# Performance work log

Hardware: AMD Instinct MI355X
Metric: run time of the kernel (lower is better)

The kernel has to match this reference:

```python
import jax, jax.numpy as jnp
import numpy as np

N_NODES = 50000
N_EDGES = 800000
D = 64
N_REL = 16


def setup_inputs() -> dict:
    key = jax.random.key(0)
    ks = jax.random.split(key, 8)
    return {
        "nfeat": jax.random.normal(ks[0], (N_NODES, D), dtype=jnp.float32),
        "efeat": jax.random.normal(ks[1], (N_EDGES, D), dtype=jnp.float32),
        "relation_W": jax.random.normal(ks[2], (N_REL, D, D), dtype=jnp.float32) * (1.0 / np.sqrt(D)),
        "W1": jax.random.normal(ks[3], (D, D), dtype=jnp.float32) * (1.0 / np.sqrt(D)),
        "W2": jax.random.normal(ks[4], (D, D), dtype=jnp.float32) * (1.0 / np.sqrt(D)),
        "src": jax.random.randint(ks[5], (N_EDGES,), 0, N_NODES, dtype=jnp.int32),
        "dst": jax.random.randint(ks[6], (N_EDGES,), 0, N_NODES, dtype=jnp.int32),
        "etype": jax.random.randint(ks[7], (N_EDGES,), 0, N_REL, dtype=jnp.int32),
    }


def _leaky_relu(x, slope=0.01):
    return jnp.where(x >= 0, x, slope * x)


def reference(nfeat, efeat, relation_W, W1, W2, src, dst, etype):
    N, Din = nfeat.shape
    R, _, Dr = relation_W.shape
    # W_r h for every (relation, node) pair, then gather per-edge.
    # Mathematically identical to per-edge bmm_maybe_select, but avoids the
    # (E, Din, Dr) per-edge weight materialization.
    proj = jnp.einsum('nd,rde->rne', nfeat, relation_W).reshape(R * N, Dr)  # (R*N, Dr)
    flat_src = etype * N + src
    flat_dst = etype * N + dst
    t_r = proj[flat_src]  # (E, Dr) == W_r h_t
    h_r = proj[flat_dst]  # (E, Dr) == W_r h_h
    # att = (W_r h_t)^T tanh(W_r h_h + e_r)
    att = jnp.sum(t_r * jnp.tanh(h_r + efeat), axis=-1)  # (E,)
    # edge softmax grouped by destination node
    seg_max = jax.ops.segment_max(att, dst, num_segments=N)  # (N,)
    ex = jnp.exp(att - seg_max[dst])
    denom = jax.ops.segment_sum(ex, dst, num_segments=N)  # (N,)
    a = ex / denom[dst]  # (E,)
    # u_mul_e + sum scatter aggregation
    h_neighbor = jax.ops.segment_sum(nfeat[src] * a[:, None], dst, num_segments=N)  # (N, Din)
    # Bi-interaction residual
    out = _leaky_relu((nfeat + h_neighbor) @ W1) + _leaky_relu((nfeat * h_neighbor) @ W2)
    return (h_neighbor, out)
```

## Files before the change

kernel.cpp:

```cpp
#include <hip/hip_runtime.h>
#include <math.h>


#define DIM 64
#define PA 72

typedef _Float16 half8 __attribute__((ext_vector_type(8)));
typedef float f32x4 __attribute__((ext_vector_type(4)));
typedef unsigned int u32x4 __attribute__((ext_vector_type(4)));

__device__ __forceinline__ float4 f4zero() { return make_float4(0.f, 0.f, 0.f, 0.f); }

__device__ __forceinline__ unsigned short f2bf(float x) {
    unsigned u = __float_as_uint(x);
    u += 0x7FFFu + ((u >> 16) & 1u);
    return (unsigned short)(u >> 16);
}

__device__ __forceinline__ float fast_tanh(float x) {
    float ex = __expf(2.0f * x);
    return 1.0f - 2.0f / (ex + 1.0f);
}

__device__ __forceinline__ void bf8up(u32x4 u, float* f) {
    f[0] = __uint_as_float(u[0] << 16);
    f[1] = __uint_as_float(u[0] & 0xFFFF0000u);
    f[2] = __uint_as_float(u[1] << 16);
    f[3] = __uint_as_float(u[1] & 0xFFFF0000u);
    f[4] = __uint_as_float(u[2] << 16);
    f[5] = __uint_as_float(u[2] & 0xFFFF0000u);
    f[6] = __uint_as_float(u[3] << 16);
    f[7] = __uint_as_float(u[3] & 0xFFFF0000u);
}

__global__ __launch_bounds__(256) void k_proj(const float* __restrict__ nfeat,
                                              const float* __restrict__ relW,
                                              unsigned short* __restrict__ proj,
                                              int N, int R) {
    __shared__ _Float16 shA[64 * PA];
    __shared__ _Float16 shB[64 * PA];

    const int tx = threadIdx.x;
    const int n0 = blockIdx.x * 64;

    const float4* nf4 = (const float4*)(nfeat + (size_t)n0 * DIM);
#pragma unroll
    for (int i = 0; i < 4; ++i) {
        int idx = tx + 256 * i;
        int row = idx >> 4, c = idx & 15;
        float4 v = (n0 + row < N) ? nf4[idx] : f4zero();
        _Float16* p = &shA[row * PA + c * 4];
        p[0] = (_Float16)v.x; p[1] = (_Float16)v.y;
        p[2] = (_Float16)v.z; p[3] = (_Float16)v.w;
    }
    __syncthreads();

    const int w = tx >> 6;
    const int lane = tx & 63;
    const int lm = lane & 15;
    const int lq = lane >> 4;
    const int m0 = w * 16;

    half8 a0 = *(const half8*)&shA[(m0 + lm) * PA + 0 * 32 + lq * 8];
    half8 a1 = *(const half8*)&shA[(m0 + lm) * PA + 1 * 32 + lq * 8];

    for (int r = 0; r < R; ++r) {
        __syncthreads();
        const float4* Wr4 = (const float4*)(relW + (size_t)r * DIM * DIM);
#pragma unroll
        for (int i = 0; i < 4; ++i) {
            int idx = tx + 256 * i;
            int d = idx >> 4, c = (idx & 15) * 4;
            float4 v = Wr4[idx];
            shB[(c + 0) * PA + d] = (_Float16)v.x;
            shB[(c + 1) * PA + d] = (_Float16)v.y;
            shB[(c + 2) * PA + d] = (_Float16)v.z;
            shB[(c + 3) * PA + d] = (_Float16)v.w;
        }
        __syncthreads();

        f32x4 acc[4];
#pragma unroll
        for (int ct = 0; ct < 4; ++ct) {
            half8 b0 = *(const half8*)&shB[(ct * 16 + lm) * PA + 0 * 32 + lq * 8];
            half8 b1 = *(const half8*)&shB[(ct * 16 + lm) * PA + 1 * 32 + lq * 8];
            f32x4 c = {0.f, 0.f, 0.f, 0.f};
            c = __builtin_amdgcn_mfma_f32_16x16x32_f16(a0, b0, c, 0, 0, 0);
            c = __builtin_amdgcn_mfma_f32_16x16x32_f16(a1, b1, c, 0, 0, 0);
            acc[ct] = c;
        }

        unsigned short* projR = proj + ((size_t)r * N + n0) * DIM;
#pragma unroll
        for (int ct = 0; ct < 4; ++ct) {
#pragma unroll
            for (int i = 0; i < 4; ++i) {
                int row = m0 + lq * 4 + i;
                int col = ct * 16 + lm;
                if (n0 + row < N)
                    projR[(size_t)row * DIM + col] = f2bf(acc[ct][i]);
            }
        }
    }
}

__global__ __launch_bounds__(256) void k_hist(const int* __restrict__ dst,
                                              int* __restrict__ deg, int E) {
    int e = blockIdx.x * 256 + threadIdx.x;
    if (e < E) atomicAdd(&deg[dst[e]], 1);
}

__global__ __launch_bounds__(256) void k_scan1(const int* __restrict__ deg,
                                               int* __restrict__ bsum, int N) {
    __shared__ int sh[256];
    int i = blockIdx.x * 256 + threadIdx.x;
    int t = threadIdx.x;
    sh[t] = (i < N) ? deg[i] : 0;
    __syncthreads();
#pragma unroll
    for (int s = 128; s > 0; s >>= 1) {
        if (t < s) sh[t] += sh[t + s];
        __syncthreads();
    }
    if (t == 0) bsum[blockIdx.x] = sh[0];
}

__global__ __launch_bounds__(256) void k_scan2(int* __restrict__ bsum, int nb,
                                               int* __restrict__ offN, int E) {
    __shared__ int sh[256];
    int t = threadIdx.x;
    int v = (t < nb) ? bsum[t] : 0;
    sh[t] = v;
    __syncthreads();
#pragma unroll
    for (int d = 1; d < 256; d <<= 1) {
        int o = (t >= d) ? sh[t - d] : 0;
        __syncthreads();
        sh[t] += o;
        __syncthreads();
    }
    if (t < nb) bsum[t] = sh[t] - v;
    if (t == 0) offN[0] = E;
}

__global__ __launch_bounds__(256) void k_scan3(const int* __restrict__ deg,
                                               const int* __restrict__ bsum,
                                               int* __restrict__ off,
                                               int* __restrict__ cursor, int N) {
    __shared__ int sh[256];
    int i = blockIdx.x * 256 + threadIdx.x;
    int t = threadIdx.x;
    int v = (i < N) ? deg[i] : 0;
    sh[t] = v;
    __syncthreads();
#pragma unroll
    for (int d = 1; d < 256; d <<= 1) {
        int o = (t >= d) ? sh[t - d] : 0;
        __syncthreads();
        sh[t] += o;
        __syncthreads();
    }
    if (i < N) {
        int pre = bsum[blockIdx.x] + sh[t] - v;
        off[i] = pre;
        cursor[i] = pre;
    }
}

__global__ __launch_bounds__(256) void k_fill(const int* __restrict__ dst,
                                              const int* __restrict__ src,
                                              int* __restrict__ cursor,
                                              int* __restrict__ pos,
                                              int* __restrict__ src_s, int E) {
    int e = blockIdx.x * 256 + threadIdx.x;
    if (e >= E) return;
    int p = atomicAdd(&cursor[dst[e]], 1);
    pos[e] = p;
    src_s[p] = src[e];
}

__global__ __launch_bounds__(256) void k_att(const unsigned short* __restrict__ proj,
                                             const float* __restrict__ efeat,
                                             const int* __restrict__ src,
                                             const int* __restrict__ dst,
                                             const int* __restrict__ etype,
                                             const int* __restrict__ pos,
                                             float* __restrict__ att_s,
                                             int N, int E) {
    int t = blockIdx.x * 256 + threadIdx.x;
    int e = t >> 3;
    int sub = t & 7;
    if (e >= E) return;
    int s = src[e], d = dst[e], r = etype[e];

    const u32x4* tp = (const u32x4*)(proj + ((size_t)((unsigned)(r * N + s))) * DIM) + sub;
    const u32x4* hp = (const u32x4*)(proj + ((size_t)((unsigned)(r * N + d))) * DIM) + sub;
    const f32x4* ef = (const f32x4*)(efeat + (size_t)e * DIM) + sub * 2;

    u32x4 tu = *tp;
    u32x4 hu = *hp;
    f32x4 efa = __builtin_nontemporal_load(ef);
    f32x4 efb = __builtin_nontemporal_load(ef + 1);

    float tf[8], hf[8];
    bf8up(tu, tf);
    bf8up(hu, hf);
    float ev[8] = {efa[0], efa[1], efa[2], efa[3], efb[0], efb[1], efb[2], efb[3]};

    float dotv = 0.f;
#pragma unroll
    for (int i = 0; i < 8; ++i)
        dotv = fmaf(tf[i], fast_tanh(hf[i] + ev[i]), dotv);

    dotv += __shfl_xor(dotv, 1);
    dotv += __shfl_xor(dotv, 2);
    dotv += __shfl_xor(dotv, 4);

    if (sub == 0) att_s[pos[e]] = dotv;
}

__global__ __launch_bounds__(256) void k_aggB(const float* __restrict__ att_s,
                                              const int* __restrict__ src_s,
                                              const float* __restrict__ nfeat,
                                              const int* __restrict__ off,
                                              const float* __restrict__ W1,
                                              const float* __restrict__ W2,
                                              float* __restrict__ hn,
                                              float* __restrict__ out,
                                              int N) {
    const int node = blockIdx.x * 4 + (threadIdx.x >> 6);
    if (node >= N) return;
    const int lane = threadIdx.x & 63;

    const int jb = off[node];
    const int je = off[node + 1];

    float m = -INFINITY;
    for (int j0 = jb; j0 < je; j0 += 64) {
        int j = j0 + lane;
        float a = (j < je) ? att_s[j] : -INFINITY;
        m = fmaxf(m, a);
    }
#pragma unroll
    for (int ms = 32; ms; ms >>= 1) m = fmaxf(m, __shfl_xor(m, ms));

    float pl = 0.f, acc = 0.f, acc2 = 0.f;
    for (int j0 = jb; j0 < je; j0 += 64) {
        int j = j0 + lane;
        int cnt = min(64, je - j0);
        float a = (j < je) ? att_s[j] : -INFINITY;
        float p = __expf(a - m);
        int s = (j < je) ? src_s[j] : 0;
        pl += p;
        int jj = 0;
        for (; jj + 3 < cnt; jj += 4) {
            float pj0 = __shfl(p, jj + 0);
            float pj1 = __shfl(p, jj + 1);
            float pj2 = __shfl(p, jj + 2);
            float pj3 = __shfl(p, jj + 3);
            int sj0 = __shfl(s, jj + 0);
            int sj1 = __shfl(s, jj + 1);
            int sj2 = __shfl(s, jj + 2);
            int sj3 = __shfl(s, jj + 3);
            float x0 = nfeat[(size_t)sj0 * DIM + lane];
            float x1 = nfeat[(size_t)sj1 * DIM + lane];
            float x2 = nfeat[(size_t)sj2 * DIM + lane];
            float x3 = nfeat[(size_t)sj3 * DIM + lane];
            acc  = fmaf(pj0, x0, acc);
            acc2 = fmaf(pj1, x1, acc2);
            acc  = fmaf(pj2, x2, acc);
            acc2 = fmaf(pj3, x3, acc2);
        }
        for (; jj < cnt; ++jj) {
            float pj = __shfl(p, jj);
            int sj = __shfl(s, jj);
            acc = fmaf(pj, nfeat[(size_t)sj * DIM + lane], acc);
        }
    }
    acc += acc2;
#pragma unroll
    for (int ms = 32; ms; ms >>= 1) pl += __shfl_xor(pl, ms);

    const float hval = (je > jb) ? acc / pl : 0.f;
    hn[(size_t)node * DIM + lane] = hval;

    const float nf = nfeat[(size_t)node * DIM + lane];
    const float v1 = nf + hval;
    const float v2 = nf * hval;
    float o1 = 0.f, o2 = 0.f;
#pragma unroll 8
    for (int d = 0; d < DIM; ++d) {
        float s1 = __shfl(v1, d);
        float s2 = __shfl(v2, d);
        o1 = fmaf(s1, W1[d * DIM + lane], o1);
        o2 = fmaf(s2, W2[d * DIM + lane], o2);
    }
    out[(size_t)node * DIM + lane] =
        (o1 >= 0.f ? o1 : 0.01f * o1) + (o2 >= 0.f ? o2 : 0.01f * o2);
}

extern "C" void kernel_launch(void* const* d_in, const int* in_sizes, int n_in,
                              void* d_out, int out_size, void* d_ws, size_t ws_size,
                              hipStream_t stream) {
    const float* nfeat = (const float*)d_in[0];
    const float* efeat = (const float*)d_in[1];
    const float* relW  = (const float*)d_in[2];
    const float* W1    = (const float*)d_in[3];
    const float* W2    = (const float*)d_in[4];
    const int* src   = (const int*)d_in[5];
    const int* dst   = (const int*)d_in[6];
    const int* etype = (const int*)d_in[7];

    const int N = in_sizes[0] / DIM;
    const int E = in_sizes[5];
    const int R = in_sizes[2] / (DIM * DIM);
    const int NB = (N + 255) / 256;

    float* out = (float*)d_out;
    float* hn  = out;
    float* bi  = out + (size_t)N * DIM;

    unsigned short* proj = (unsigned short*)d_ws;
    size_t projElems = (size_t)R * N * DIM;
    int* deg    = (int*)(proj + projElems);
    int* off    = deg + N;
    int* cursor = off + (N + 1);
    int* bsum   = cursor + N;
    int* pos    = bsum + 256;
    int* src_s  = pos + E;
    float* att_s = (float*)(src_s + E);

    (void)hipMemsetAsync(deg, 0, (size_t)N * sizeof(int), stream);

    k_hist<<<(E + 255) / 256, 256, 0, stream>>>(dst, deg, E);
    k_scan1<<<NB, 256, 0, stream>>>(deg, bsum, N);
    k_scan2<<<1, 256, 0, stream>>>(bsum, NB, off + N, E);
    k_scan3<<<NB, 256, 0, stream>>>(deg, bsum, off, cursor, N);
    k_fill<<<(E + 255) / 256, 256, 0, stream>>>(dst, src, cursor, pos, src_s, E);

    k_proj<<<(N + 63) / 64, 256, 0, stream>>>(nfeat, relW, proj, N, R);

    k_att<<<((size_t)E * 8 + 255) / 256, 256, 0, stream>>>(proj, efeat, src, dst, etype,
                                                           pos, att_s, N, E);

    k_aggB<<<(N + 3) / 4, 256, 0, stream>>>(att_s, src_s, nfeat, off,
                                            W1, W2, hn, bi, N);
}
```

Measured before the change: 567.3 us.

## Fuse CSR fill into histogram ranks, coalesce proj stores, cache bi-interaction weights in LDS

New measurement: 568.2 us. Within noise of the previous version (+0.2%).

```diff
diff --git a/kernel.cpp b/kernel.cpp
--- a/kernel.cpp
+++ b/kernel.cpp
@@ -39,6 +39,7 @@
                                               int N, int R) {
     __shared__ _Float16 shA[64 * PA];
     __shared__ _Float16 shB[64 * PA];
+    unsigned short* shSt = (unsigned short*)shA;
 
     const int tx = threadIdx.x;
     const int n0 = blockIdx.x * 64;
@@ -90,63 +91,39 @@
             acc[ct] = c;
         }
 
-        unsigned short* projR = proj + ((size_t)r * N + n0) * DIM;
 #pragma unroll
         for (int ct = 0; ct < 4; ++ct) {
 #pragma unroll
             for (int i = 0; i < 4; ++i) {
                 int row = m0 + lq * 4 + i;
                 int col = ct * 16 + lm;
-                if (n0 + row < N)
-                    projR[(size_t)row * DIM + col] = f2bf(acc[ct][i]);
+                shSt[row * PA + col] = f2bf(acc[ct][i]);
             }
         }
+        __syncthreads();
+
+        unsigned short* projR = proj + ((size_t)r * N + n0) * DIM;
+#pragma unroll
+        for (int k = 0; k < 2; ++k) {
+            int chunk = tx + k * 256;
+            int row = chunk >> 3, cc = chunk & 7;
+            uint4 v = *(const uint4*)&shSt[row * PA + cc * 8];
+            if (n0 + row < N)
+                *(uint4*)&projR[(size_t)row * DIM + cc * 8] = v;
+        }
     }
 }
 
 __global__ __launch_bounds__(256) void k_hist(const int* __restrict__ dst,
-                                              int* __restrict__ deg, int E) {
+                                              int* __restrict__ deg,
+                                              int* __restrict__ rank, int E) {
     int e = blockIdx.x * 256 + threadIdx.x;
-    if (e < E) atomicAdd(&deg[dst[e]], 1);
+    if (e < E) rank[e] = atomicAdd(&deg[dst[e]], 1);
 }
 
 __global__ __launch_bounds__(256) void k_scan1(const int* __restrict__ deg,
+                                               int* __restrict__ epart,
                                                int* __restrict__ bsum, int N) {
-    __shared__ int sh[256];
-    int i = blockIdx.x * 256 + threadIdx.x;
-    int t = threadIdx.x;
-    sh[t] = (i < N) ? deg[i] : 0;
-    __syncthreads();
-#pragma unroll
-    for (int s = 128; s > 0; s >>= 1) {
-        if (t < s) sh[t] += sh[t + s];
-        __syncthreads();
-    }
-    if (t == 0) bsum[blockIdx.x] = sh[0];
-}
-
-__global__ __launch_bounds__(256) void k_scan2(int* __restrict__ bsum, int nb,
-                                               int* __restrict__ offN, int E) {
-    __shared__ int sh[256];
-    int t = threadIdx.x;
-    int v = (t < nb) ? bsum[t] : 0;
-    sh[t] = v;
-    __syncthreads();
-#pragma unroll
-    for (int d = 1; d < 256; d <<= 1) {
-        int o = (t >= d) ? sh[t - d] : 0;
-        __syncthreads();
-        sh[t] += o;
-        __syncthreads();
-    }
-    if (t < nb) bsum[t] = sh[t] - v;
-    if (t == 0) offN[0] = E;
-}
-
-__global__ __launch_bounds__(256) void k_scan3(const int* __restrict__ deg,
-                                               const int* __restrict__ bsum,
-                                               int* __restrict__ off,
-                                               int* __restrict__ cursor, int N) {
     __shared__ int sh[256];
     int i = blockIdx.x * 256 + threadIdx.x;
     int t = threadIdx.x;
@@ -160,23 +137,36 @@
         sh[t] += o;
         __syncthreads();
     }
-    if (i < N) {
-        int pre = bsum[blockIdx.x] + sh[t] - v;
-        off[i] = pre;
-        cursor[i] = pre;
-    }
-}
-
-__global__ __launch_bounds__(256) void k_fill(const int* __restrict__ dst,
-                                              const int* __restrict__ src,
-                                              int* __restrict__ cursor,
-                                              int* __restrict__ pos,
-                                              int* __restrict__ src_s, int E) {
-    int e = blockIdx.x * 256 + threadIdx.x;
-    if (e >= E) return;
-    int p = atomicAdd(&cursor[dst[e]], 1);
-    pos[e] = p;
-    src_s[p] = src[e];
+    if (i < N) epart[i] = sh[t] - v;
+    if (t == 255) bsum[blockIdx.x] = sh[255];
+}
+
+__global__ __launch_bounds__(1024) void k_scan2(const int* __restrict__ epart,
+                                                const int* __restrict__ bsum,
+                                                int nb,
+                                                int* __restrict__ off,
+                                                int N, int E) {
+    __shared__ int bx[256];
+    int t = threadIdx.x;
+    int v = 0;
+    if (t < 256) {
+        v = (t < nb) ? bsum[t] : 0;
+        bx[t] = v;
+    }
+    __syncthreads();
+#pragma unroll
+    for (int d = 1; d < 256; d <<= 1) {
+        int o = 0;
+        if (t < 256 && t >= d) o = bx[t - d];
+        __syncthreads();
+        if (t < 256) bx[t] += o;
+        __syncthreads();
+    }
+    if (t < 256) bx[t] -= v;
+    __syncthreads();
+    for (int i = t; i < N; i += 1024)
+        off[i] = epart[i] + bx[i >> 8];
+    if (t == 0) off[N] = E;
 }
 
 __global__ __launch_bounds__(256) void k_att(const unsigned short* __restrict__ proj,
@@ -184,8 +174,10 @@
                                              const int* __restrict__ src,
                                              const int* __restrict__ dst,
                                              const int* __restrict__ etype,
-                                             const int* __restrict__ pos,
+                                             const int* __restrict__ rank,
+                                             const int* __restrict__ off,
                                              float* __restrict__ att_s,
+                                             int* __restrict__ src_s,
                                              int N, int E) {
     int t = blockIdx.x * 256 + threadIdx.x;
     int e = t >> 3;
@@ -216,7 +208,9 @@
     dotv += __shfl_xor(dotv, 2);
     dotv += __shfl_xor(dotv, 4);
 
-    if (sub == 0) att_s[pos[e]] = dotv;
+    int p = off[d] + rank[e];
+    if (sub == 0) att_s[p] = dotv;
+    if (sub == 1) src_s[p] = s;
 }
 
 __global__ __launch_bounds__(256) void k_aggB(const float* __restrict__ att_s,
@@ -228,9 +222,24 @@
                                               float* __restrict__ hn,
                                               float* __restrict__ out,
                                               int N) {
-    const int node = blockIdx.x * 4 + (threadIdx.x >> 6);
+    __shared__ float shW[2][DIM * DIM];
+    const int tx = threadIdx.x;
+    {
+        const float4* w14 = (const float4*)W1;
+        const float4* w24 = (const float4*)W2;
+        float4* s0 = (float4*)shW[0];
+        float4* s1 = (float4*)shW[1];
+#pragma unroll
+        for (int i = 0; i < 4; ++i) {
+            s0[tx + 256 * i] = w14[tx + 256 * i];
+            s1[tx + 256 * i] = w24[tx + 256 * i];
+        }
+    }
+    __syncthreads();
+
+    const int node = blockIdx.x * 4 + (tx >> 6);
     if (node >= N) return;
-    const int lane = threadIdx.x & 63;
+    const int lane = tx & 63;
 
     const int jb = off[node];
     const int je = off[node + 1];
@@ -292,8 +301,8 @@
     for (int d = 0; d < DIM; ++d) {
         float s1 = __shfl(v1, d);
         float s2 = __shfl(v2, d);
-        o1 = fmaf(s1, W1[d * DIM + lane], o1);
-        o2 = fmaf(s2, W2[d * DIM + lane], o2);
+        o1 = fmaf(s1, shW[0][d * DIM + lane], o1);
+        o2 = fmaf(s2, shW[1][d * DIM + lane], o2);
     }
     out[(size_t)node * DIM + lane] =
         (o1 >= 0.f ? o1 : 0.01f * o1) + (o2 >= 0.f ? o2 : 0.01f * o2);
@@ -324,24 +333,22 @@
     size_t projElems = (size_t)R * N * DIM;
     int* deg    = (int*)(proj + projElems);
     int* off    = deg + N;
-    int* cursor = off + (N + 1);
-    int* bsum   = cursor + N;
-    int* pos    = bsum + 256;
-    int* src_s  = pos + E;
+    int* epart  = off + (N + 1);
+    int* bsum   = epart + N;
+    int* rank   = bsum + 256;
+    int* src_s  = rank + E;
     float* att_s = (float*)(src_s + E);
 
     (void)hipMemsetAsync(deg, 0, (size_t)N * sizeof(int), stream);
 
-    k_hist<<<(E + 255) / 256, 256, 0, stream>>>(dst, deg, E);
-    k_scan1<<<NB, 256, 0, stream>>>(deg, bsum, N);
-    k_scan2<<<1, 256, 0, stream>>>(bsum, NB, off + N, E);
-    k_scan3<<<NB, 256, 0, stream>>>(deg, bsum, off, cursor, N);
-    k_fill<<<(E + 255) / 256, 256, 0, stream>>>(dst, src, cursor, pos, src_s, E);
+    k_hist<<<(E + 255) / 256, 256, 0, stream>>>(dst, deg, rank, E);
+    k_scan1<<<NB, 256, 0, stream>>>(deg, epart, bsum, N);
+    k_scan2<<<1, 1024, 0, stream>>>(epart, bsum, NB, off, N, E);
 
     k_proj<<<(N + 63) / 64, 256, 0, stream>>>(nfeat, relW, proj, N, R);
 
     k_att<<<((size_t)E * 8 + 255) / 256, 256, 0, stream>>>(proj, efeat, src, dst, etype,
-                                                           pos, att_s, N, E);
+                                                           rank, off, att_s, src_s, N, E);
 
     k_aggB<<<(N + 3) / 4, 256, 0, stream>>>(att_s, src_s, nfeat, off,
                                             W1, W2, hn, bi, N);
```
